# Performance work log

Measured on AMD Instinct MI355X. Metric: run time of the kernel, lower is better.

## Reference

```python
import jax, jax.numpy as jnp
import numpy as np

D_MODEL = 1024
N_HEAD = 16
D_HEAD = 64
D_CAT = N_HEAD * D_HEAD
HD_MLP = 4096
LN_EPS = 1e-5


def setup_inputs() -> dict:
    key = jax.random.key(0)
    ks = jax.random.split(key, 12)
    bn, t = 2, 2048
    s = lambda fan_in: 1.0 / np.sqrt(fan_in)
    return {
        "x": jax.random.normal(ks[0], (bn, t, D_MODEL), dtype=jnp.float32),
        "mask": jnp.ones((bn, t), dtype=jnp.int32),
        "w_qkv": jax.random.normal(ks[1], (D_MODEL, 3 * D_CAT), dtype=jnp.float32) * s(D_MODEL),
        "w_tail": jax.random.normal(ks[2], (D_CAT, D_MODEL), dtype=jnp.float32) * s(D_CAT),
        "b_tail": jnp.zeros((D_MODEL,), dtype=jnp.float32),
        "ln1_g": jnp.ones((D_MODEL,), dtype=jnp.float32),
        "ln1_b": jnp.zeros((D_MODEL,), dtype=jnp.float32),
        "ln2_g": jnp.ones((D_MODEL,), dtype=jnp.float32),
        "ln2_b": jnp.zeros((D_MODEL,), dtype=jnp.float32),
        "w1": jax.random.normal(ks[3], (D_MODEL, HD_MLP), dtype=jnp.float32) * s(D_MODEL),
        "b1": jnp.zeros((HD_MLP,), dtype=jnp.float32),
        "w2": jax.random.normal(ks[4], (HD_MLP, D_MODEL), dtype=jnp.float32) * s(HD_MLP),
        "b2": jnp.zeros((D_MODEL,), dtype=jnp.float32),
    }


def _layer_norm(x, g, b):
    mu = jnp.mean(x, axis=-1, keepdims=True)
    var = jnp.mean(jnp.square(x - mu), axis=-1, keepdims=True)
    return (x - mu) * jax.lax.rsqrt(var + LN_EPS) * g + b


def _attention(z, mask, w_qkv, w_tail, b_tail):
    bn, t, _ = z.shape
    qkv = z @ w_qkv                      # (bn, t, 3*d_cat)
    qkv = qkv.reshape(bn, t, N_HEAD, 3, D_HEAD)  # chunk layout: per-head [q|k|v]
    q = qkv[..., 0, :].transpose(0, 2, 1, 3)     # (bn, h, t, dh)
    k = qkv[..., 1, :].transpose(0, 2, 1, 3)
    v = qkv[..., 2, :].transpose(0, 2, 1, 3)
    scale = D_HEAD ** -0.5
    dots = jnp.einsum("bhqd,bhkd->bhqk", q, k) * scale
    key_mask = (mask == 0)[:, None, None, :]     # (bn,1,1,t)
    dots = jnp.where(key_mask, -jnp.inf, dots)
    coef = jax.nn.softmax(dots, axis=-1)
    attn = jnp.einsum("bhqk,bhkd->bhqd", coef, v)
    out = attn.transpose(0, 2, 1, 3).reshape(bn, t, D_CAT)
    return out @ w_tail + b_tail


def reference(x, mask, w_qkv, w_tail, b_tail, ln1_g, ln1_b, ln2_g, ln2_b, w1, b1, w2, b2):
    z = _layer_norm(x, ln1_g, ln1_b)
    x = _attention(z, mask, w_qkv, w_tail, b_tail) + x
    z = _layer_norm(x, ln2_g, ln2_b)
    h = jax.nn.gelu(z @ w1 + b1, approximate=False)  # torch GELU default = exact erf
    x = h @ w2 + b2 + x
    return x
```

## Files before the change

### kernel.cpp

```cpp
#include <hip/hip_runtime.h>
#include <hip/hip_bf16.h>

#define DM 1024
#define TT 2048
#define NH 16
#define DH 64
#define HD 4096

typedef __attribute__((ext_vector_type(4))) float f32x4;
typedef __attribute__((ext_vector_type(8))) short s16x8;
typedef __attribute__((ext_vector_type(4))) short s16x4;

static __device__ __forceinline__ short f2bf(float f) {
  __hip_bfloat16 h = __float2bfloat16(f);
  return *reinterpret_cast<short*>(&h);
}

typedef const __attribute__((address_space(1))) char* gas1_t;
typedef __attribute__((address_space(3))) char* las3_t;
static __device__ __forceinline__ void glds16(const void* g, void* l) {
  __builtin_amdgcn_global_load_lds((gas1_t)g, (las3_t)l, 16, 0, 0);
}

__global__ __launch_bounds__(256) void transpose_cvt_k(
    const float* __restrict__ in, short* __restrict__ out, int K, int N)
{
  __shared__ float tile[32][33];
  const int n0 = blockIdx.x * 32, k0 = blockIdx.y * 32;
  const int tx = threadIdx.x & 31, ty = threadIdx.x >> 5;
#pragma unroll
  for (int i = 0; i < 4; ++i)
    tile[ty + i * 8][tx] = in[(size_t)(k0 + ty + i * 8) * N + n0 + tx];
  __syncthreads();
#pragma unroll
  for (int i = 0; i < 4; ++i) {
    int n = ty + i * 8;
    out[(size_t)(n0 + n) * K + k0 + tx] = f2bf(tile[tx][n]);
  }
}

__global__ __launch_bounds__(256) void ln_k(
    const float* __restrict__ x, const float* __restrict__ g,
    const float* __restrict__ b, short* __restrict__ out)
{
  const int row = blockIdx.x;
  const int tid = threadIdx.x;
  const float4 v = ((const float4*)(x + (size_t)row * DM))[tid];
  float s = v.x + v.y + v.z + v.w;
  float q = v.x * v.x + v.y * v.y + v.z * v.z + v.w * v.w;
#pragma unroll
  for (int off = 1; off < 64; off <<= 1) {
    s += __shfl_xor(s, off);
    q += __shfl_xor(q, off);
  }
  __shared__ float ss[4], sq[4];
  const int wave = tid >> 6;
  if ((tid & 63) == 0) { ss[wave] = s; sq[wave] = q; }
  __syncthreads();
  s = ss[0] + ss[1] + ss[2] + ss[3];
  q = sq[0] + sq[1] + sq[2] + sq[3];
  const float mu = s * (1.0f / DM);
  const float var = q * (1.0f / DM) - mu * mu;
  const float rs = rsqrtf(var + 1e-5f);
  const float4 gv = ((const float4*)g)[tid];
  const float4 bv = ((const float4*)b)[tid];
  s16x4 o;
  o[0] = f2bf((v.x - mu) * rs * gv.x + bv.x);
  o[1] = f2bf((v.y - mu) * rs * gv.y + bv.y);
  o[2] = f2bf((v.z - mu) * rs * gv.z + bv.z);
  o[3] = f2bf((v.w - mu) * rs * gv.w + bv.w);
  *(s16x4*)(out + (size_t)row * DM + tid * 4) = o;
}

template<int EPI, int BN>
__global__ __launch_bounds__(256) void gemm_bt(
    const short* __restrict__ A, const short* __restrict__ B,
    const float* __restrict__ bias, const float* __restrict__ res,
    float* __restrict__ outF, short* __restrict__ outB,
    short* __restrict__ outK, short* __restrict__ outV,
    int M, int N, int K)
{
  constexpr int MR = (BN == 128) ? 4 : 2;
  __shared__ short As[2][128 * 32];
  __shared__ short Bs[2][BN * 32];
  const int tid = threadIdx.x;
  const int wave = tid >> 6, lane = tid & 63;
  const int l15 = lane & 15, lhi = lane >> 4;
  const int bm = blockIdx.x, bn = blockIdx.y;
  const int wr = (BN == 128) ? (wave >> 1) : wave;
  const int wc = (BN == 128) ? (wave & 1) : 0;
  f32x4 acc[MR][4] = {};

  const int sr = wave * 16 + (lane >> 2);
  const int schunk = ((lane & 3) ^ ((lane >> 3) & 3)) * 16;
  const char* gA = (const char*)(A + (size_t)(bm * 128 + sr) * K) + schunk;
  const char* gB = (const char*)(B + (size_t)(bn * BN + sr) * K) + schunk;
  const size_t rowstep = (size_t)64 * K * 2;

  const int NK = K >> 5;
  const int rsw = (l15 >> 1) & 3;
  const int achunk = (lhi ^ rsw) << 4;

  auto stage = [&](int buf, int kt) {
    const size_t koff = (size_t)kt * 64;
    char* lA = (char*)As[buf] + wave * 1024;
    glds16(gA + koff, lA);
    glds16(gA + koff + rowstep, lA + 4096);
    char* lB = (char*)Bs[buf] + wave * 1024;
    glds16(gB + koff, lB);
    if (BN == 128) glds16(gB + koff + rowstep, lB + 4096);
  };

  stage(0, 0);
  __syncthreads();
  int cur = 0;
  for (int kt = 0; kt < NK; ++kt) {
    if (kt + 1 < NK) stage(cur ^ 1, kt + 1);
    s16x8 af[MR], bfv[4];
#pragma unroll
    for (int m = 0; m < MR; ++m) {
      const int row = wr * (MR * 16) + m * 16 + l15;
      af[m] = *(const s16x8*)((const char*)As[cur] + row * 64 + achunk);
    }
#pragma unroll
    for (int n = 0; n < 4; ++n) {
      const int row = wc * 64 + n * 16 + l15;
      bfv[n] = *(const s16x8*)((const char*)Bs[cur] + row * 64 + achunk);
    }
#pragma unroll
    for (int m = 0; m < MR; ++m)
#pragma unroll
      for (int n = 0; n < 4; ++n)
        acc[m][n] = __builtin_amdgcn_mfma_f32_16x16x32_bf16(af[m], bfv[n], acc[m][n], 0, 0, 0);
    __syncthreads();
    cur ^= 1;
  }

  const int rowb = bm * 128 + wr * (MR * 16);
  const int colb = bn * BN + wc * 64;
#pragma unroll
  for (int m = 0; m < MR; ++m) {
#pragma unroll
    for (int n = 0; n < 4; ++n) {
      if (EPI == 3) {
        const int col0 = colb + n * 16;
        const int h = col0 / 192;
        const int c0 = col0 - h * 192;
        const int region = c0 >> 6;
        const int d = (c0 & 63) + l15;
        const int row0 = rowb + m * 16 + lhi * 4;
        const int bb = row0 >> 11, tl0 = row0 & 2047;
        const size_t bh = (size_t)bb * NH + h;
        if (region == 2) {
          s16x4 pk;
#pragma unroll
          for (int rr = 0; rr < 4; ++rr) pk[rr] = f2bf(acc[m][n][rr]);
          *(s16x4*)(outV + (bh * 64 + d) * TT + tl0) = pk;
        } else {
          short* dst = (region == 0) ? outB : outK;
          const float qs = (region == 0) ? 0.18033688011112042f : 1.0f;
#pragma unroll
          for (int rr = 0; rr < 4; ++rr)
            dst[(bh * TT + tl0 + rr) * 64 + d] = f2bf(acc[m][n][rr] * qs);
        }
      } else {
        const int col = colb + n * 16 + l15;
        const float bv = bias[col];
#pragma unroll
        for (int rr = 0; rr < 4; ++rr) {
          const int row = rowb + m * 16 + lhi * 4 + rr;
          float v = acc[m][n][rr] + bv;
          if (EPI == 1) v += res[(size_t)row * N + col];
          if (EPI == 2) v = 0.5f * v * (1.0f + erff(v * 0.70710678118f));
          if (EPI == 1) outF[(size_t)row * N + col] = v;
          else outB[(size_t)row * N + col] = f2bf(v);
        }
      }
    }
  }
}

#define PSTRIDE 144
#define PFRAG   2304
__global__ __launch_bounds__(256, 4) void attn_k(
    const short* __restrict__ Qb, const short* __restrict__ Kb,
    const short* __restrict__ Vtb, const int* __restrict__ mask,
    short* __restrict__ outp)
{
  const int tid = threadIdx.x, wave = tid >> 6, lane = tid & 63;
  const int l15 = lane & 15, lhi = lane >> 4;
  const int lb = blockIdx.x;
  const int bh = lb & 31, qb = lb >> 5;
  const int b = bh >> 4, h = bh & 15;
  const int qw = qb * 64 + wave * 16;

  __shared__ short Ks[64 * 64];
  __shared__ short Vt[64 * 64];
  __shared__ char Ps[4 * PFRAG];

  const short* qp = Qb + ((size_t)bh * TT + qw + l15) * 64;
  const s16x8 aq0 = *(const s16x8*)(qp + lhi * 8);
  const s16x8 aq1 = *(const s16x8*)(qp + 32 + lhi * 8);

  f32x4 o[4] = {};
  float mrow = -1e30f, lrow = 0.f;

  const int kr_s = tid >> 2, kc_s = (tid & 3) * 16;
  const int ksw = (kr_s & 7) << 4;

  const short* kgb = Kb + (size_t)bh * TT * 64 + (size_t)kr_s * 64 + kc_s;
  const short* vgb = Vtb + ((size_t)bh * 64 + kr_s) * TT + kc_s;

  s16x8 kpre[2], vpre[2];
  kpre[0] = *(const s16x8*)kgb;       kpre[1] = *(const s16x8*)(kgb + 8);
  vpre[0] = *(const s16x8*)vgb;       vpre[1] = *(const s16x8*)(vgb + 8);
  int m0 = mask[b * TT + lane];

  char* pb = Ps + wave * PFRAG + l15 * PSTRIDE;

  for (int t0 = 0; t0 < TT; t0 += 64) {
    char* krow = (char*)Ks + kr_s * 128;
    *(s16x8*)(krow + ((kc_s * 2) ^ ksw)) = kpre[0];
    *(s16x8*)(krow + ((kc_s * 2 + 16) ^ ksw)) = kpre[1];
    char* vrow = (char*)Vt + kr_s * 128;
    *(s16x8*)(vrow + ((kc_s * 2) ^ ksw)) = vpre[0];
    *(s16x8*)(vrow + ((kc_s * 2 + 16) ^ ksw)) = vpre[1];
    __syncthreads();

    const unsigned long long mb0 = __ballot(m0 != 0);
    const bool full = mb0 == ~0ULL;

    if (t0 + 64 < TT) {
      const short* kg = kgb + (size_t)(t0 + 64) * 64;
      const short* vg = vgb + t0 + 64;
      kpre[0] = *(const s16x8*)kg;  kpre[1] = *(const s16x8*)(kg + 8);
      vpre[0] = *(const s16x8*)vg;  vpre[1] = *(const s16x8*)(vg + 8);
      m0 = mask[b * TT + t0 + 64 + lane];
    }

    f32x4 sv[4];
    __builtin_amdgcn_s_setprio(1);
#pragma unroll
    for (int n = 0; n < 4; ++n) {
      const int row = n * 16 + l15;
      const int sw = (row & 7) << 4;
      const char* kr = (const char*)Ks + row * 128;
      const s16x8 a0 = *(const s16x8*)(kr + ((lhi * 16) ^ sw));
      const s16x8 a1 = *(const s16x8*)(kr + ((64 + lhi * 16) ^ sw));
      f32x4 z = {};
      z = __builtin_amdgcn_mfma_f32_16x16x32_bf16(a0, aq0, z, 0, 0, 0);
      z = __builtin_amdgcn_mfma_f32_16x16x32_bf16(a1, aq1, z, 0, 0, 0);
      sv[n] = z;
    }
    __builtin_amdgcn_s_setprio(0);

    if (!full) {
#pragma unroll
      for (int n = 0; n < 4; ++n) {
        const unsigned nib = (unsigned)(mb0 >> (n * 16 + lhi * 4)) & 0xF;
#pragma unroll
        for (int rr = 0; rr < 4; ++rr)
          if (!((nib >> rr) & 1)) sv[n][rr] = -3e38f;
      }
    }

    float mx0 = fmaxf(sv[0][0], sv[1][0]), mx1 = fmaxf(sv[0][1], sv[1][1]);
    float mx2 = fmaxf(sv[0][2], sv[1][2]), mx3 = fmaxf(sv[0][3], sv[1][3]);
    mx0 = fmaxf(mx0, fmaxf(sv[2][0], sv[3][0]));
    mx1 = fmaxf(mx1, fmaxf(sv[2][1], sv[3][1]));
    mx2 = fmaxf(mx2, fmaxf(sv[2][2], sv[3][2]));
    mx3 = fmaxf(mx3, fmaxf(sv[2][3], sv[3][3]));
    float mx = fmaxf(fmaxf(mx0, mx1), fmaxf(mx2, mx3));
    mx = fmaxf(mx, __shfl_xor(mx, 16));
    mx = fmaxf(mx, __shfl_xor(mx, 32));
    if (__any(mx > mrow + 8.0f)) {
      const float mn = fmaxf(mrow, mx);
      const float alpha = exp2f(mrow - mn);
      mrow = mn;
      lrow *= alpha;
      float ar[4];
#pragma unroll
      for (int rr = 0; rr < 4; ++rr) ar[rr] = __shfl(alpha, lhi * 4 + rr);
#pragma unroll
      for (int db = 0; db < 4; ++db)
#pragma unroll
        for (int rr = 0; rr < 4; ++rr) o[db][rr] *= ar[rr];
    }
    float s0 = 0.f, s1 = 0.f, s2 = 0.f, s3 = 0.f;
#pragma unroll
    for (int n = 0; n < 4; ++n) {
      sv[n][0] = exp2f(sv[n][0] - mrow); s0 += sv[n][0];
      sv[n][1] = exp2f(sv[n][1] - mrow); s1 += sv[n][1];
      sv[n][2] = exp2f(sv[n][2] - mrow); s2 += sv[n][2];
      sv[n][3] = exp2f(sv[n][3] - mrow); s3 += sv[n][3];
    }
    float sum = (s0 + s1) + (s2 + s3);
    sum += __shfl_xor(sum, 16);
    sum += __shfl_xor(sum, 32);
    lrow += sum;

#pragma unroll
    for (int n = 0; n < 4; ++n) {
      s16x4 pk;
#pragma unroll
      for (int rr = 0; rr < 4; ++rr) pk[rr] = f2bf(sv[n][rr]);
      *(s16x4*)(pb + n * 32 + lhi * 8) = pk;
    }
    asm volatile("s_waitcnt lgkmcnt(0)" ::: "memory");
    __builtin_amdgcn_sched_barrier(0);
    s16x8 ap[2];
    ap[0] = *(const s16x8*)(pb + lhi * 16);
    ap[1] = *(const s16x8*)(pb + 64 + lhi * 16);

    __builtin_amdgcn_s_setprio(1);
#pragma unroll
    for (int db = 0; db < 4; ++db) {
      const int d = db * 16 + l15;
      const int swv = (d & 7) << 4;
      const char* vr2 = (const char*)Vt + d * 128;
#pragma unroll
      for (int ks = 0; ks < 2; ++ks) {
        const s16x8 bv = *(const s16x8*)(vr2 + ((ks * 64 + lhi * 16) ^ swv));
        o[db] = __builtin_amdgcn_mfma_f32_16x16x32_bf16(ap[ks], bv, o[db], 0, 0, 0);
      }
    }
    __builtin_amdgcn_s_setprio(0);
    __syncthreads();
  }

  float lr[4];
#pragma unroll
  for (int rr = 0; rr < 4; ++rr) lr[rr] = __shfl(lrow, lhi * 4 + rr);
#pragma unroll
  for (int db = 0; db < 4; ++db) {
#pragma unroll
    for (int rr = 0; rr < 4; ++rr) {
      const int qg = qw + lhi * 4 + rr;
      const int cg = h * 64 + db * 16 + l15;
      outp[(size_t)(b * TT + qg) * DM + cg] = f2bf(o[db][rr] / lr[rr]);
    }
  }
}

extern "C" void kernel_launch(void* const* d_in, const int* in_sizes, int n_in,
                              void* d_out, int out_size, void* d_ws, size_t ws_size,
                              hipStream_t stream)
{
  const float* x      = (const float*)d_in[0];
  const int*   mask   = (const int*)d_in[1];
  const float* w_qkv  = (const float*)d_in[2];
  const float* w_tail = (const float*)d_in[3];
  const float* b_tail = (const float*)d_in[4];
  const float* ln1g   = (const float*)d_in[5];
  const float* ln1b   = (const float*)d_in[6];
  const float* ln2g   = (const float*)d_in[7];
  const float* ln2b   = (const float*)d_in[8];
  const float* w1     = (const float*)d_in[9];
  const float* b1     = (const float*)d_in[10];
  const float* w2     = (const float*)d_in[11];
  const float* b2     = (const float*)d_in[12];

  char* ws = (char*)d_ws;
  size_t off = 0;
  auto take = [&](size_t bytes) {
    char* p = ws + off;
    off += (bytes + 255) & ~(size_t)255;
    return p;
  };
  short* slotW = (short*)take((size_t)4096 * 2048 * 2);
  short* slotZ = (short*)take((size_t)4096 * 1024 * 2);
  short* qb    = (short*)take((size_t)32 * 2048 * 64 * 2);
  short* kb    = (short*)take((size_t)32 * 2048 * 64 * 2);
  short* vtb   = (short*)take((size_t)32 * 64 * 2048 * 2);
  float* x1    = (float*)take((size_t)4096 * 1024 * 4);
  short* hbuf  = (short*)take((size_t)4096 * 4096 * 2);

  transpose_cvt_k<<<dim3(3072 / 32, 1024 / 32), 256, 0, stream>>>(w_qkv, slotW, 1024, 3072);
  ln_k<<<4096, 256, 0, stream>>>(x, ln1g, ln1b, slotZ);
  gemm_bt<3, 128><<<dim3(32, 24), 256, 0, stream>>>(slotZ, slotW, nullptr, nullptr,
                                                    nullptr, qb, kb, vtb, 4096, 3072, 1024);
  attn_k<<<1024, 256, 0, stream>>>(qb, kb, vtb, mask, slotZ);
  transpose_cvt_k<<<dim3(1024 / 32, 1024 / 32), 256, 0, stream>>>(w_tail, slotW, 1024, 1024);
  gemm_bt<1, 64><<<dim3(32, 16), 256, 0, stream>>>(slotZ, slotW, b_tail, x,
                                                   x1, nullptr, nullptr, nullptr, 4096, 1024, 1024);
  ln_k<<<4096, 256, 0, stream>>>(x1, ln2g, ln2b, slotZ);
  transpose_cvt_k<<<dim3(4096 / 32, 1024 / 32), 256, 0, stream>>>(w1, slotW, 1024, 4096);
  gemm_bt<2, 128><<<dim3(32, 32), 256, 0, stream>>>(slotZ, slotW, b1, nullptr,
                                                    nullptr, hbuf, nullptr, nullptr, 4096, 4096, 1024);
  transpose_cvt_k<<<dim3(1024 / 32, 4096 / 32), 256, 0, stream>>>(w2, slotW, 4096, 1024);
  gemm_bt<1, 64><<<dim3(32, 16), 256, 0, stream>>>(hbuf, slotW, b2, x1,
                                                   (float*)d_out, nullptr, nullptr, nullptr, 4096, 1024, 4096);
}
```

Before: 285.8 us.

## Add double-buffered 512-thread pipelined GEMM for MLP up and down projections

Introduces a new gemm_pipe kernel using 128x128 tiles, 8 waves, double-buffered LDS staged via global_load_lds with swizzled layout, and explicit vmcnt waits so loads of the next K-tile overlap MFMA work. The MLP up-projection (with GELU epilogue) and down-projection (with bias+residual) now use it, the latter with larger 128-column tiles (fewer blocks). The GELU branch is removed from the old gemm_bt epilogue since it is no longer used there. Risks lower occupancy from 64KB LDS and fewer blocks for the N=1024 GEMM.

```diff
diff --git a/kernel.cpp b/kernel.cpp
--- a/kernel.cpp
+++ b/kernel.cpp
@@ -171,9 +171,101 @@
           const int row = rowb + m * 16 + lhi * 4 + rr;
           float v = acc[m][n][rr] + bv;
           if (EPI == 1) v += res[(size_t)row * N + col];
-          if (EPI == 2) v = 0.5f * v * (1.0f + erff(v * 0.70710678118f));
           if (EPI == 1) outF[(size_t)row * N + col] = v;
           else outB[(size_t)row * N + col] = f2bf(v);
+        }
+      }
+    }
+  }
+}
+
+template<int EPI>
+__global__ __launch_bounds__(512, 4) void gemm_pipe(
+    const short* __restrict__ A, const short* __restrict__ B,
+    const float* __restrict__ bias, const float* __restrict__ res,
+    float* __restrict__ outF, short* __restrict__ outB,
+    int M, int N, int K)
+{
+  __shared__ short As[2][2][64 * 64];
+  __shared__ short Bs[2][2][64 * 64];
+  static_assert(sizeof(short) * 64 * 64 == 128 * 64, "plane = 128 rows x 64B");
+  const int tid = threadIdx.x;
+  const int wave = tid >> 6, lane = tid & 63;
+  const int l15 = lane & 15, lhi = lane >> 4;
+  const int bm = blockIdx.x, bn = blockIdx.y;
+  const int wr = wave >> 2;
+  const int wc = wave & 3;
+  f32x4 acc[4][2] = {};
+
+  const int srow = tid >> 2;
+  const int scs = ((tid & 3) ^ ((srow >> 1) & 3)) * 16;
+  const int ldst = srow * 64 + (tid & 3) * 16;
+  const char* gA = (const char*)(A + (size_t)(bm * 128 + srow) * K);
+  const char* gB = (const char*)(B + (size_t)(bn * 128 + srow) * K);
+
+  const int NT = K >> 6;
+
+  auto stagePair = [&](int buf, int kt, int kh) {
+    const size_t go = (size_t)kt * 128 + kh * 64 + scs;
+    glds16(gA + go, (char*)As[buf][kh] + ldst);
+    glds16(gB + go, (char*)Bs[buf][kh] + ldst);
+  };
+
+  stagePair(0, 0, 0);
+  stagePair(0, 0, 1);
+
+  int buf = 0;
+  for (int t = 0; t < NT; ++t) {
+#pragma unroll
+    for (int kh = 0; kh < 2; ++kh) {
+      const bool more = (t + 1 < NT);
+      if (more || kh == 0) asm volatile("s_waitcnt vmcnt(2)" ::: "memory");
+      else                 asm volatile("s_waitcnt vmcnt(0)" ::: "memory");
+      __builtin_amdgcn_s_barrier();
+      __builtin_amdgcn_sched_barrier(0);
+      s16x8 af[4], bfv[2];
+#pragma unroll
+      for (int m = 0; m < 4; ++m) {
+        const int row = wr * 64 + m * 16 + l15;
+        af[m] = *(const s16x8*)((const char*)As[buf][kh] + row * 64 +
+                                ((lhi ^ ((row >> 1) & 3)) << 4));
+      }
+#pragma unroll
+      for (int n = 0; n < 2; ++n) {
+        const int row = wc * 32 + n * 16 + l15;
+        bfv[n] = *(const s16x8*)((const char*)Bs[buf][kh] + row * 64 +
+                                 ((lhi ^ ((row >> 1) & 3)) << 4));
+      }
+      if (more) stagePair(buf ^ 1, t + 1, kh);
+      __builtin_amdgcn_s_setprio(1);
+#pragma unroll
+      for (int m = 0; m < 4; ++m)
+#pragma unroll
+        for (int n = 0; n < 2; ++n)
+          acc[m][n] = __builtin_amdgcn_mfma_f32_16x16x32_bf16(af[m], bfv[n], acc[m][n], 0, 0, 0);
+      __builtin_amdgcn_s_setprio(0);
+    }
+    buf ^= 1;
+  }
+
+  const int rowb = bm * 128 + wr * 64;
+  const int colb = bn * 128 + wc * 32;
+#pragma unroll
+  for (int m = 0; m < 4; ++m) {
+#pragma unroll
+    for (int n = 0; n < 2; ++n) {
+      const int col = colb + n * 16 + l15;
+      const float bv = bias[col];
+#pragma unroll
+      for (int rr = 0; rr < 4; ++rr) {
+        const int row = rowb + m * 16 + lhi * 4 + rr;
+        float v = acc[m][n][rr] + bv;
+        if (EPI == 1) {
+          v += res[(size_t)row * N + col];
+          outF[(size_t)row * N + col] = v;
+        } else {
+          v = 0.5f * v * (1.0f + erff(v * 0.70710678118f));
+          outB[(size_t)row * N + col] = f2bf(v);
         }
       }
     }
@@ -385,9 +477,9 @@
                                                    x1, nullptr, nullptr, nullptr, 4096, 1024, 1024);
   ln_k<<<4096, 256, 0, stream>>>(x1, ln2g, ln2b, slotZ);
   transpose_cvt_k<<<dim3(4096 / 32, 1024 / 32), 256, 0, stream>>>(w1, slotW, 1024, 4096);
-  gemm_bt<2, 128><<<dim3(32, 32), 256, 0, stream>>>(slotZ, slotW, b1, nullptr,
-                                                    nullptr, hbuf, nullptr, nullptr, 4096, 4096, 1024);
+  gemm_pipe<2><<<dim3(32, 32), 512, 0, stream>>>(slotZ, slotW, b1, nullptr,
+                                                 nullptr, hbuf, 4096, 4096, 1024);
   transpose_cvt_k<<<dim3(1024 / 32, 4096 / 32), 256, 0, stream>>>(w2, slotW, 4096, 1024);
-  gemm_bt<1, 64><<<dim3(32, 16), 256, 0, stream>>>(hbuf, slotW, b2, x1,
-                                                   (float*)d_out, nullptr, nullptr, nullptr, 4096, 1024, 4096);
-}
+  gemm_pipe<1><<<dim3(32, 8), 512, 0, stream>>>(hbuf, slotW, b2, x1,
+                                                (float*)d_out, nullptr, 4096, 1024, 4096);
+}
```

New measurement: 265.7 us. 7.0% less time.
